# Optimization experiments

Measured on AMD Instinct MI355X. Metric: run time of the kernel, lower is better.

Reference implementation:

```python
import jax, jax.numpy as jnp
import numpy as np


def conv3d(x, w, b, stride=(1, 1, 1)):
    # x: (B,C,D,H,W), w: (O,I,3,3,3), padding 1 on all three dims (PyTorch Conv3d k=3,p=1)
    y = jax.lax.conv_general_dilated(
        x, w, stride, [(1, 1)] * 3,
        dimension_numbers=("NCDHW", "OIDHW", "NCDHW"))
    return y + b[None, :, None, None, None]


def deconv3d(x, w, b):
    # ConvTranspose3d with k=3, s=1, p=1 == conv with spatially flipped kernel
    return conv3d(x, jnp.flip(w, axis=(2, 3, 4)), b)


def upsample2x(x):
    # nn.Upsample(scale_factor=(1,2,2), mode='nearest')
    return jnp.repeat(jnp.repeat(x, 2, axis=3), 2, axis=4)


def fo_pool(z, f, reverse):
    # linear gated recurrence h_t = f_t*h_{t-1} + (1-f_t)*z_t along band axis (dim 2)
    zt = jnp.moveaxis(z, 2, 0)
    ft = jnp.moveaxis(f, 2, 0)
    if reverse:
        zt, ft = zt[::-1], ft[::-1]

    def step(h, zf):
        zi, fi = zf
        h = fi * h + (1.0 - fi) * zi
        return h, h

    _, hs = jax.lax.scan(step, jnp.zeros_like(zt[0]), (zt, ft))
    if reverse:
        hs = hs[::-1]
    return jnp.moveaxis(hs, 0, 2)


def qrnn(gates, reverse):
    z, f = jnp.split(gates, 2, axis=1)
    return fo_pool(jnp.tanh(z), jax.nn.sigmoid(f), reverse)


def biqrnn(gates):
    z, f1, f2 = jnp.split(gates, 3, axis=1)
    z = jnp.tanh(z)
    return (fo_pool(z, jax.nn.sigmoid(f1), False)
            + fo_pool(z, jax.nn.sigmoid(f2), True))


def _forward(x, fe_w, fe_b, e0_w, e0_b, e1_w, e1_b, e2_w, e2_b, e3_w, e3_b,
             e4_w, e4_b, d0_w, d0_b, d1_w, d1_b, d2_w, d2_b, d3_w, d3_b,
             d4_w, d4_b, rec_w, rec_b):
    # feature extractor: BiQRNNConv3D(1 -> 16), gates 48ch
    fe = biqrnn(conv3d(x, fe_w, fe_b))                        # (B,16,31,256,256)
    # encoder (alternating direction: F,T,F,T,F)
    e0 = qrnn(conv3d(fe, e0_w, e0_b), False)                  # 16ch @256
    e1 = qrnn(conv3d(e0, e1_w, e1_b, stride=(1, 2, 2)), True) # 32ch @128
    e2 = qrnn(conv3d(e1, e2_w, e2_b), False)                  # 32ch @128
    e3 = qrnn(conv3d(e2, e3_w, e3_b, stride=(1, 2, 2)), True) # 64ch @64
    e4 = qrnn(conv3d(e3, e4_w, e4_b), False)                  # 64ch @64
    # decoder (reverse starts at True after encoder toggles)
    d0 = qrnn(deconv3d(e4, d0_w, d0_b), True)                 # 64ch @64
    d1 = qrnn(conv3d(upsample2x(d0 + e3), d1_w, d1_b), False) # 32ch @128
    d2 = qrnn(deconv3d(d1 + e2, d2_w, d2_b), True)            # 32ch @128
    d3 = qrnn(conv3d(upsample2x(d2 + e1), d3_w, d3_b), False) # 16ch @256
    d4 = qrnn(deconv3d(d3 + e0, d4_w, d4_b), True)            # 16ch @256
    out = d4 + fe
    # reconstructor: BiQRNNDeConv3D(16 -> 1), act='tanh'
    out = biqrnn(deconv3d(out, rec_w, rec_b))                 # (B,1,31,256,256)
    return out + x


def setup_inputs() -> dict:
    key = jax.random.key(0)
    ks = jax.random.split(key, 26)

    def W(k, o, i):
        return jax.random.normal(k, (o, i, 3, 3, 3), jnp.float32) * 0.05

    def Bv(k, o):
        return jax.random.normal(k, (o,), jnp.float32) * 0.01

    x = jax.random.normal(ks[0], (1, 1, 31, 256, 256), jnp.float32)
    inp = {"x": x}
    shapes = {
        "fe": (48, 1), "e0": (32, 16), "e1": (64, 16), "e2": (64, 32),
        "e3": (128, 32), "e4": (128, 64), "d0": (128, 64), "d1": (64, 64),
        "d2": (64, 32), "d3": (32, 32), "d4": (32, 16), "rec": (3, 16),
    }
    for j, (name, (o, i)) in enumerate(shapes.items()):
        inp[name + "_w"] = W(ks[1 + 2 * j], o, i)
        inp[name + "_b"] = Bv(ks[2 + 2 * j], o)
    return inp


def reference(x, fe_w, fe_b, e0_w, e0_b, e1_w, e1_b, e2_w, e2_b, e3_w, e3_b,
              e4_w, e4_b, d0_w, d0_b, d1_w, d1_b, d2_w, d2_b, d3_w, d3_b,
              d4_w, d4_b, rec_w, rec_b):
    return _forward(x, fe_w, fe_b, e0_w, e0_b, e1_w, e1_b, e2_w, e2_b,
                    e3_w, e3_b, e4_w, e4_b, d0_w, d0_b, d1_w, d1_b,
                    d2_w, d2_b, d3_w, d3_b, d4_w, d4_b, rec_w, rec_b)
```

## Files before the change

### kernel.cpp

```cpp
#include <hip/hip_runtime.h>
#include <hip/hip_bf16.h>
#include <cstdint>
#include <cstddef>

using f16 = _Float16;
typedef _Float16 f16x2 __attribute__((ext_vector_type(2)));
typedef _Float16 f16x8 __attribute__((ext_vector_type(8)));
typedef float f32x4 __attribute__((ext_vector_type(4)));

static constexpr int DD = 31;
static constexpr long long U  = 31LL * 256 * 256;
static constexpr long long V2 = 31LL * 128 * 128;
static constexpr long long POOL_UNITS = 56;
static constexpr int CP_CHUNK = 16;

union U32H2 { unsigned u; f16x2 h; };

__device__ __forceinline__ float toF(float v) { return v; }
__device__ __forceinline__ float toF(f16 v) { return (float)v; }
__device__ __forceinline__ void stv(float* p, float v) { *p = v; }
__device__ __forceinline__ void stv(f16* p, float v) { *p = (f16)v; }
__device__ __forceinline__ float sigm(float x) { return 1.f / (1.f + __expf(-x)); }

__device__ __forceinline__ unsigned packh2(float a, float b)
{
    U32H2 r; r.h = f16x2{(f16)a, (f16)b}; return r.u;
}
__device__ __forceinline__ unsigned addh2(unsigned a, unsigned b)
{
    U32H2 x, y, r; x.u = a; y.u = b; r.h = x.h + y.h; return r.u;
}
__device__ __forceinline__ float dot2f(unsigned v, unsigned w, float c)
{
#if __has_builtin(__builtin_amdgcn_fdot2)
    U32H2 uv, uw; uv.u = v; uw.u = w;
    return __builtin_amdgcn_fdot2(uv.h, uw.h, c, false);
#else
    U32H2 uv, uw; uv.u = v; uw.u = w;
    c = fmaf((float)uv.h.x, (float)uw.h.x, c);
    return fmaf((float)uv.h.y, (float)uw.h.y, c);
#endif
}

__global__ __launch_bounds__(256)
void fill_k(f16* p, long long n)
{
    const long long stride = (long long)gridDim.x * 256;
    for (long long i = (long long)blockIdx.x * 256 + threadIdx.x; i < n; i += stride)
        p[i] = (f16)0.f;
}

__global__ __launch_bounds__(256)
void pack_w_k(const float* __restrict__ wt, f16* __restrict__ outp,
              int CIN, int nCo, int flip)
{
    const int e = blockIdx.x * 256 + threadIdx.x;
    const int nhg = (nCo + 7) >> 3;
    const int total = (CIN >> 3) * nhg * 9 * 64;
    if (e >= total) return;
    const int l = e & 63;
    const int r = e >> 6;
    const int r9 = r % 9;
    const int t2 = r / 9;
    const int hg = t2 % nhg;
    const int cc = t2 / nhg;
    const int kd = r9 / 3, Tg = r9 - kd * 3;
    const int n = hg * 8 + (l & 15);
    const int T = Tg * 4 + (l >> 4);
    f16x8 bv;
#pragma unroll
    for (int i = 0; i < 8; ++i) bv[i] = (f16)0.f;
    if (T <= 8 && n < nCo) {
        const int kh = T / 3, kw = T - (T / 3) * 3;
        const int st = flip ? ((2 - kd) * 9 + (2 - kh) * 3 + (2 - kw))
                            : (kd * 9 + kh * 3 + kw);
        const size_t wb8 = ((size_t)n * CIN + cc * 8) * 27 + st;
#pragma unroll
        for (int i = 0; i < 8; ++i)
            bv[i] = (f16)wt[wb8 + (size_t)i * 27];
    }
    *(f16x8*)(outp + (size_t)e * 8) = bv;
}

template<int STRIDE, bool FLIP, int CIN, int HOUT, int WOUT, int NT, bool PACKED,
         bool OUTIL>
__global__ __launch_bounds__(256)
void conv_mfma_k(const f16* __restrict__ in, const float* __restrict__ wt,
                 const f16x8* __restrict__ wb, const float* __restrict__ bias,
                 f16* __restrict__ out, int nCo, int cg0, int nhg)
{
    constexpr int CIC = CIN / 8;
    constexpr int HIN = HOUT * STRIDE, WIN = WOUT * STRIDE;
    constexpr int WT = (WOUT > 128) ? 128 : WOUT;
    constexpr int RR = 128 / WT;
    constexpr int COLS = WOUT / WT;
    constexpr int TPD = (HOUT / RR) * COLS;
    constexpr int AH = STRIDE * (RR - 1) + 3;
    constexpr int AW = STRIDE * (WT - 1) + 3;
    constexpr int APOS = 3 * AH * AW;
    constexpr int NBENT = NT * 576;

    extern __shared__ unsigned lds[];
    unsigned* Alds = lds;
    unsigned* Blds = lds + APOS * 4;

    const int tid = threadIdx.x;
    const int l = tid & 63;
    const int wid = tid >> 6;

    const int bx = blockIdx.x;
    const int d0 = bx / TPD;
    const int rem = bx - d0 * TPD;
    const int h0 = (rem / COLS) * RR;
    const int wb_ = (rem % COLS) * WT;

    const int co_base = blockIdx.y * (16 * NT);
    const int nRem = nCo - co_base;
    const int hgBase = cg0 + blockIdx.y * (2 * NT);

    const int base_h = STRIDE * h0 - 1;
    const int base_w = STRIDE * wb_ - 1;
    constexpr size_t HWin = (size_t)HIN * WIN;
    constexpr size_t DHW = (size_t)DD * HWin;
    const unsigned* inu = (const unsigned*)in;

    int hho[2], wlo[2];
#pragma unroll
    for (int mt = 0; mt < 2; ++mt) {
        const int p = wid * 32 + mt * 16 + (l & 15);
        hho[mt] = p / WT;
        wlo[mt] = p - hho[mt] * WT;
    }
    const int g = l >> 4;
    int khg[3], kwg[3];
#pragma unroll
    for (int Tg = 0; Tg < 3; ++Tg) {
        int T = Tg * 4 + g;
        if (T > 8) T = 8;
        khg[Tg] = T / 3;
        kwg[Tg] = T - (T / 3) * 3;
    }

    f32x4 acc[2][NT];
#pragma unroll
    for (int mt = 0; mt < 2; ++mt)
#pragma unroll
        for (int nt = 0; nt < NT; ++nt)
            acc[mt][nt] = (f32x4){0.f, 0.f, 0.f, 0.f};

    for (int cc = 0; cc < CIC; ++cc) {
        f16x8 bfr[NT][9];
        if (PACKED) {
#pragma unroll
            for (int nt = 0; nt < NT; ++nt)
#pragma unroll
                for (int r9 = 0; r9 < 9; ++r9)
                    bfr[nt][r9] = wb[((size_t)cc * nhg + hgBase + nt * 2) * 9 * 64
                                     + (size_t)r9 * 64 + l];
        }
        __syncthreads();
        for (int t = tid; t < APOS; t += 256) {
            const int ww = t % AW;
            const int t2 = t / AW;
            const int hh = t2 % AH;
            const int dd = t2 / AH;
            const int d = d0 - 1 + dd;
            const int h = base_h + hh;
            const int w = base_w + ww;
            uint4 val = make_uint4(0u, 0u, 0u, 0u);
            if ((unsigned)d < (unsigned)DD && (unsigned)h < (unsigned)HIN &&
                (unsigned)w < (unsigned)WIN) {
                const size_t gi = (size_t)(cc * 4) * DHW +
                                  (size_t)d * HWin + (size_t)h * WIN + w;
                val.x = inu[gi];
                val.y = inu[gi + DHW];
                val.z = inu[gi + 2 * DHW];
                val.w = inu[gi + 3 * DHW];
            }
            *(uint4*)(Alds + (size_t)t * 4) = val;
        }
        if (!PACKED) {
            for (int t = tid; t < NBENT; t += 256) {
                const int ll = t & 63;
                const int f = t >> 6;
                const int nt = f / 9;
                const int r9 = f - nt * 9;
                const int kd = r9 / 3;
                const int Tg = r9 - kd * 3;
                const int n = nt * 16 + (ll & 15);
                const int gg = ll >> 4;
                const int T = Tg * 4 + gg;
                f16x8 bv;
                if (T <= 8 && n < nRem) {
                    const int kh = T / 3, kw = T - (T / 3) * 3;
                    const int st = FLIP ? ((2 - kd) * 9 + (2 - kh) * 3 + (2 - kw))
                                        : (kd * 9 + kh * 3 + kw);
                    const size_t wb8 = ((size_t)(co_base + n) * CIN + cc * 8) * 27 + st;
#pragma unroll
                    for (int e = 0; e < 8; ++e)
                        bv[e] = (f16)wt[wb8 + (size_t)e * 27];
                } else {
#pragma unroll
                    for (int e = 0; e < 8; ++e) bv[e] = (f16)0.f;
                }
                *(f16x8*)(Blds + (size_t)t * 4) = bv;
            }
        }
        __syncthreads();
#pragma unroll
        for (int kd = 0; kd < 3; ++kd) {
#pragma unroll
            for (int Tg = 0; Tg < 3; ++Tg) {
                f16x8 bfrag[NT];
#pragma unroll
                for (int nt = 0; nt < NT; ++nt)
                    bfrag[nt] = PACKED ? bfr[nt][kd * 3 + Tg]
                                       : *(const f16x8*)
                        (Blds + (size_t)(((nt * 9) + kd * 3 + Tg) * 64 + l) * 4);
                const int kh = khg[Tg], kw = kwg[Tg];
#pragma unroll
                for (int mt = 0; mt < 2; ++mt) {
                    const int hh = STRIDE * hho[mt] + kh;
                    const int ww = STRIDE * wlo[mt] + kw;
                    const f16x8 afrag = *(const f16x8*)
                        (Alds + (size_t)((kd * AH + hh) * AW + ww) * 4);
#pragma unroll
                    for (int nt = 0; nt < NT; ++nt)
                        acc[mt][nt] = __builtin_amdgcn_mfma_f32_16x16x32_f16(
                            afrag, bfrag[nt], acc[mt][nt], 0, 0, 0);
                }
            }
        }
    }

    const int n = l & 15;
#pragma unroll
    for (int nt = 0; nt < NT; ++nt) {
        const int ng = nt * 16 + n;
        if (ng < nRem) {
            const int co = co_base + ng;
            const float bv = bias[co];
#pragma unroll
            for (int mt = 0; mt < 2; ++mt) {
#pragma unroll
                for (int r = 0; r < 4; ++r) {
                    const int p = wid * 32 + mt * 16 + (l >> 4) * 4 + r;
                    const int hh = p / WT;
                    const int wl = p - hh * WT;
                    const int h = h0 + hh, w = wb_ + wl;
                    const float val = acc[mt][nt][r] + bv;
                    if (OUTIL) {
                        const size_t coPlane =
                            (size_t)(co >> 1) * DD * HOUT * WOUT * 2 + (co & 1);
                        out[coPlane + ((size_t)d0 * HOUT + h) * WOUT * 2 +
                            (size_t)w * 2] = (f16)val;
                    } else {
                        out[((size_t)co * DD + d0) * HOUT * WOUT +
                            (size_t)h * WOUT + w] = (f16)val;
                    }
                }
            }
        }
    }
}

template<int CIN, int HLO, int WLO, int NT>
__global__ __launch_bounds__(256)
void conv_mfma_up_k(const f16* __restrict__ ia, const f16* __restrict__ ib,
                    const f16x8* __restrict__ wb, const float* __restrict__ bias,
                    f16* __restrict__ out, int nCo, int cg0, int nhg)
{
    constexpr int CIC = CIN / 8;
    constexpr int HOUT = 2 * HLO, WOUT = 2 * WLO;
    constexpr int WT = (WOUT > 128) ? 128 : WOUT;
    constexpr int COLS = WOUT / WT;
    constexpr int TPD = HOUT * COLS;
    constexpr int AWLO = WT / 2 + 2;
    constexpr int APOS = 3 * 2 * AWLO;

    extern __shared__ unsigned lds[];

    const int tid = threadIdx.x;
    const int l = tid & 63;
    const int wid = tid >> 6;

    const int bx = blockIdx.x;
    const int d0 = bx / TPD;
    const int rem = bx - d0 * TPD;
    const int h0 = rem / COLS;
    const int wb_ = (rem % COLS) * WT;

    const int co_base = blockIdx.y * (16 * NT);
    const int nRem = nCo - co_base;
    const int hgBase = cg0 + blockIdx.y * (2 * NT);

    const int rlo0 = (h0 - 1) >> 1;
    const int clo0 = (wb_ >> 1) - 1;

    constexpr size_t HWlo = (size_t)HLO * WLO;
    constexpr size_t DHW = (size_t)DD * HWlo;
    const unsigned* iau = (const unsigned*)ia;
    const unsigned* ibu = (const unsigned*)ib;

    int wpos[2];
#pragma unroll
    for (int mt = 0; mt < 2; ++mt)
        wpos[mt] = wid * 32 + mt * 16 + (l & 15);

    const int g = l >> 4;
    int khg[3], kwg[3];
#pragma unroll
    for (int Tg = 0; Tg < 3; ++Tg) {
        int T = Tg * 4 + g;
        if (T > 8) T = 8;
        khg[Tg] = T / 3;
        kwg[Tg] = T - (T / 3) * 3;
    }

    f32x4 acc[2][NT];
#pragma unroll
    for (int mt = 0; mt < 2; ++mt)
#pragma unroll
        for (int nt = 0; nt < NT; ++nt)
            acc[mt][nt] = (f32x4){0.f, 0.f, 0.f, 0.f};

    for (int cc = 0; cc < CIC; ++cc) {
        f16x8 bfr[NT][9];
#pragma unroll
        for (int nt = 0; nt < NT; ++nt)
#pragma unroll
            for (int r9 = 0; r9 < 9; ++r9)
                bfr[nt][r9] = wb[((size_t)cc * nhg + hgBase + nt * 2) * 9 * 64
                                 + (size_t)r9 * 64 + l];
        __syncthreads();
        for (int t = tid; t < APOS; t += 256) {
            const int ww = t % AWLO;
            const int t2 = t / AWLO;
            const int rr = t2 & 1;
            const int dd = t2 >> 1;
            const int d = d0 - 1 + dd;
            const int hlo = rlo0 + rr;
            const int wlo = clo0 + ww;
            uint4 val = make_uint4(0u, 0u, 0u, 0u);
            if ((unsigned)d < (unsigned)DD && (unsigned)hlo < (unsigned)HLO &&
                (unsigned)wlo < (unsigned)WLO) {
                const size_t gi = (size_t)(cc * 4) * DHW +
                                  (size_t)d * HWlo + (size_t)hlo * WLO + wlo;
                val.x = addh2(iau[gi], ibu[gi]);
                val.y = addh2(iau[gi + DHW], ibu[gi + DHW]);
                val.z = addh2(iau[gi + 2 * DHW], ibu[gi + 2 * DHW]);
                val.w = addh2(iau[gi + 3 * DHW], ibu[gi + 3 * DHW]);
            }
            *(uint4*)(lds + (size_t)t * 4) = val;
        }
        __syncthreads();
#pragma unroll
        for (int kd = 0; kd < 3; ++kd) {
#pragma unroll
            for (int Tg = 0; Tg < 3; ++Tg) {
                const int kh = khg[Tg], kw = kwg[Tg];
                const int rr = ((h0 + kh - 1) >> 1) - rlo0;
#pragma unroll
                for (int mt = 0; mt < 2; ++mt) {
                    const int iw = ((wpos[mt] + kw - 1) >> 1) + 1;
                    const f16x8 afrag = *(const f16x8*)
                        (lds + (size_t)((kd * 2 + rr) * AWLO + iw) * 4);
#pragma unroll
                    for (int nt = 0; nt < NT; ++nt)
                        acc[mt][nt] = __builtin_amdgcn_mfma_f32_16x16x32_f16(
                            afrag, bfr[nt][kd * 3 + Tg], acc[mt][nt], 0, 0, 0);
                }
            }
        }
    }

    const int n = l & 15;
#pragma unroll
    for (int nt = 0; nt < NT; ++nt) {
        const int ng = nt * 16 + n;
        if (ng < nRem) {
            const int co = co_base + ng;
            const float bv = bias[co];
            const size_t coPlane = (size_t)(co >> 1) * DD * HOUT * WOUT * 2 + (co & 1);
#pragma unroll
            for (int mt = 0; mt < 2; ++mt) {
#pragma unroll
                for (int r = 0; r < 4; ++r) {
                    const int p = wid * 32 + mt * 16 + (l >> 4) * 4 + r;
                    out[coPlane + ((size_t)d0 * HOUT + h0) * WOUT * 2 +
                        (size_t)(wb_ + p) * 2] = (f16)(acc[mt][nt][r] + bv);
                }
            }
        }
    }
}

template<int STRIDE, bool FLIP, int CO_BLK, bool OUT_IL>
__global__ __launch_bounds__(256, 2)
void conv3d_il_k(const f16* __restrict__ in, const float* __restrict__ wt,
                 const float* __restrict__ bias, f16* __restrict__ out,
                 int Cin, int Hin, int Win, int Hout, int Wout)
{
    extern __shared__ unsigned wl2[];
    const int co_base = blockIdx.y * CO_BLK;

    const int s8 = (blockIdx.x * 256 + threadIdx.x) * 8;
    const int w0 = s8 % Wout;
    const int sh = s8 / Wout;
    const int h0 = sh % Hout;
    const int d0 = sh / Hout;

    float acc[CO_BLK][8];
#pragma unroll
    for (int j = 0; j < CO_BLK; ++j) {
        const float bv = bias[co_base + j];
#pragma unroll
        for (int o = 0; o < 8; ++o) acc[j][o] = bv;
    }

    const size_t HWin = (size_t)Hin * Win;
    const int CP = Cin >> 1;

    for (int cp0 = 0; cp0 < CP; cp0 += CP_CHUNK) {
        const int cnp = (CP - cp0 < CP_CHUNK) ? (CP - cp0) : CP_CHUNK;
        __syncthreads();
        for (int t = threadIdx.x; t < cnp * 27 * CO_BLK; t += 256) {
            const int j = t % CO_BLK;
            const int k = (t / CO_BLK) % 27;
            const int cp = t / (CO_BLK * 27);
            int src;
            if (FLIP) {
                const int kd = k / 9, kh = (k / 3) % 3, kw = k % 3;
                src = (2 - kd) * 9 + (2 - kh) * 3 + (2 - kw);
            } else {
                src = k;
            }
            const int ci = (cp0 + cp) * 2;
            const size_t wb = (size_t)(co_base + j) * Cin;
            wl2[t] = packh2(wt[(wb + ci) * 27 + src], wt[(wb + ci + 1) * 27 + src]);
        }
        __syncthreads();

        for (int cp = 0; cp < cnp; ++cp) {
            const f16* cb = in + (size_t)(cp0 + cp) * DD * HWin * 2;
            const unsigned* wc = wl2 + cp * 27 * CO_BLK;
#pragma unroll
            for (int kd = 0; kd < 3; ++kd) {
                const int di = d0 + kd - 1;
                if (di < 0 || di >= DD) continue;
#pragma unroll
                for (int kh = 0; kh < 3; ++kh) {
                    const int hi = h0 * STRIDE + kh - 1;
                    if (hi < 0 || hi >= Hin) continue;
                    const unsigned* rowu = (const unsigned*)
                        (cb + ((size_t)di * HWin + (size_t)hi * Win) * 2);
                    if (STRIDE == 1) {
                        unsigned v2[10];
                        v2[0] = (w0 > 0) ? rowu[w0 - 1] : 0u;
                        const uint4 q1 = *(const uint4*)(rowu + w0);
                        const uint4 q2 = *(const uint4*)(rowu + w0 + 4);
                        v2[1] = q1.x; v2[2] = q1.y; v2[3] = q1.z; v2[4] = q1.w;
                        v2[5] = q2.x; v2[6] = q2.y; v2[7] = q2.z; v2[8] = q2.w;
                        v2[9] = (w0 + 8 < Win) ? rowu[w0 + 8] : 0u;
                        const unsigned* wk = wc + (kd * 9 + kh * 3) * CO_BLK;
#pragma unroll
                        for (int kw = 0; kw < 3; ++kw) {
#pragma unroll
                            for (int j = 0; j < CO_BLK; ++j) {
                                const unsigned wv = wk[kw * CO_BLK + j];
#pragma unroll
                                for (int o = 0; o < 8; ++o)
                                    acc[j][o] = dot2f(v2[o + kw], wv, acc[j][o]);
                            }
                        }
                    } else {
                        unsigned v2[17];
                        const int p0 = w0 * 2;
                        v2[0] = (w0 > 0) ? rowu[p0 - 1] : 0u;
#pragma unroll
                        for (int q = 0; q < 4; ++q) {
                            const uint4 qq = *(const uint4*)(rowu + p0 + 4 * q);
                            v2[1 + 4 * q] = qq.x; v2[2 + 4 * q] = qq.y;
                            v2[3 + 4 * q] = qq.z; v2[4 + 4 * q] = qq.w;
                        }
                        const unsigned* wk = wc + (kd * 9 + kh * 3) * CO_BLK;
#pragma unroll
                        for (int kw = 0; kw < 3; ++kw) {
#pragma unroll
                            for (int j = 0; j < CO_BLK; ++j) {
                                const unsigned wv = wk[kw * CO_BLK + j];
#pragma unroll
                                for (int o = 0; o < 8; ++o)
                                    acc[j][o] = dot2f(v2[2 * o + kw], wv, acc[j][o]);
                            }
                        }
                    }
                }
            }
        }
    }

    if (OUT_IL) {
#pragma unroll
        for (int pj = 0; pj < CO_BLK / 2; ++pj) {
            f16* op = out + ((((size_t)((co_base >> 1) + pj) * DD + d0) * Hout + h0)
                             * Wout + w0) * 2;
            unsigned dw[8];
#pragma unroll
            for (int o = 0; o < 8; ++o)
                dw[o] = packh2(acc[2 * pj][o], acc[2 * pj + 1][o]);
            *(uint4*)op = make_uint4(dw[0], dw[1], dw[2], dw[3]);
            *(uint4*)(op + 8) = make_uint4(dw[4], dw[5], dw[6], dw[7]);
        }
    } else {
#pragma unroll
        for (int j = 0; j < CO_BLK; ++j) {
            f16* op = out + (((size_t)(co_base + j) * DD + d0) * Hout + h0) * Wout + w0;
            unsigned dw[4];
#pragma unroll
            for (int o = 0; o < 4; ++o)
                dw[o] = packh2(acc[j][2 * o], acc[j][2 * o + 1]);
            *(uint4*)op = make_uint4(dw[0], dw[1], dw[2], dw[3]);
        }
    }
}

template<int CO_BLK>
__global__ __launch_bounds__(256, 2)
void conv3d_up_il_k(const f16* __restrict__ ia, const f16* __restrict__ ib,
                    const float* __restrict__ wt, const float* __restrict__ bias,
                    f16* __restrict__ out, int Cin, int Hlo, int Wlo)
{
    extern __shared__ unsigned wl2[];
    const int co_base = blockIdx.y * CO_BLK;

    const int Hout = 2 * Hlo, Wout = 2 * Wlo;
    const int s8 = (blockIdx.x * 256 + threadIdx.x) * 8;
    const int w0 = s8 % Wout;
    const int sh = s8 / Wout;
    const int h0 = sh % Hout;
    const int d0 = sh / Hout;
    const int lw = w0 >> 1;

    float acc[CO_BLK][8];
#pragma unroll
    for (int j = 0; j < CO_BLK; ++j) {
        const float bv = bias[co_base + j];
#pragma unroll
        for (int o = 0; o < 8; ++o) acc[j][o] = bv;
    }
    const size_t HWlo = (size_t)Hlo * Wlo;
    const int CP = Cin >> 1;

    for (int cp0 = 0; cp0 < CP; cp0 += CP_CHUNK) {
        const int cnp = (CP - cp0 < CP_CHUNK) ? (CP - cp0) : CP_CHUNK;
        __syncthreads();
        for (int t = threadIdx.x; t < cnp * 27 * CO_BLK; t += 256) {
            const int j = t % CO_BLK;
            const int k = (t / CO_BLK) % 27;
            const int cp = t / (CO_BLK * 27);
            const int ci = (cp0 + cp) * 2;
            const size_t wb = (size_t)(co_base + j) * Cin;
            wl2[t] = packh2(wt[(wb + ci) * 27 + k], wt[(wb + ci + 1) * 27 + k]);
        }
        __syncthreads();

        for (int cp = 0; cp < cnp; ++cp) {
            const f16* cba = ia + (size_t)(cp0 + cp) * DD * HWlo * 2;
            const f16* cbb = ib + (size_t)(cp0 + cp) * DD * HWlo * 2;
            const unsigned* wc = wl2 + cp * 27 * CO_BLK;
#pragma unroll
            for (int kd = 0; kd < 3; ++kd) {
                const int di = d0 + kd - 1;
                if (di < 0 || di >= DD) continue;
#pragma unroll
                for (int kh = 0; kh < 3; ++kh) {
                    const int hi = h0 + kh - 1;
                    if (hi < 0 || hi >= Hout) continue;
                    const int hlo = hi >> 1;
                    const unsigned* rua = (const unsigned*)
                        (cba + ((size_t)di * HWlo + (size_t)hlo * Wlo) * 2);
                    const unsigned* rub = (const unsigned*)
                        (cbb + ((size_t)di * HWlo + (size_t)hlo * Wlo) * 2);
                    unsigned u[6];
                    u[0] = (lw > 0) ? addh2(rua[lw - 1], rub[lw - 1]) : 0u;
                    const uint4 qa = *(const uint4*)(rua + lw);
                    const uint4 qb = *(const uint4*)(rub + lw);
                    u[1] = addh2(qa.x, qb.x); u[2] = addh2(qa.y, qb.y);
                    u[3] = addh2(qa.z, qb.z); u[4] = addh2(qa.w, qb.w);
                    u[5] = (lw + 4 < Wlo) ? addh2(rua[lw + 4], rub[lw + 4]) : 0u;
                    const unsigned v2[10] = { u[0], u[1], u[1], u[2], u[2],
                                              u[3], u[3], u[4], u[4], u[5] };
                    const unsigned* wk = wc + (kd * 9 + kh * 3) * CO_BLK;
#pragma unroll
                    for (int kw = 0; kw < 3; ++kw) {
#pragma unroll
                        for (int j = 0; j < CO_BLK; ++j) {
                            const unsigned wv = wk[kw * CO_BLK + j];
#pragma unroll
                            for (int o = 0; o < 8; ++o)
                                acc[j][o] = dot2f(v2[o + kw], wv, acc[j][o]);
                        }
                    }
                }
            }
        }
    }
#pragma unroll
    for (int pj = 0; pj < CO_BLK / 2; ++pj) {
        f16* op = out + ((((size_t)((co_base >> 1) + pj) * DD + d0) * Hout + h0)
                         * Wout + w0) * 2;
        unsigned dw[8];
#pragma unroll
        for (int o = 0; o < 8; ++o)
            dw[o] = packh2(acc[2 * pj][o], acc[2 * pj + 1][o]);
        *(uint4*)op = make_uint4(dw[0], dw[1], dw[2], dw[3]);
        *(uint4*)(op + 8) = make_uint4(dw[4], dw[5], dw[6], dw[7]);
    }
}

__global__ __launch_bounds__(256, 2)
void conv_fe_k(const float* __restrict__ in, const float* __restrict__ wt,
               const float* __restrict__ bias, f16* __restrict__ out)
{
    __shared__ float wl[27 * 4];
    for (int t = threadIdx.x; t < 27 * 4; t += 256) {
        const int j = t % 4;
        const int k = t / 4;
        wl[t] = wt[(size_t)j * 27 + k];
    }
    __syncthreads();

    const int W = 256, H = 256;
    const int s8 = (blockIdx.x * 256 + threadIdx.x) * 8;
    const int w0 = s8 % W;
    const int sh = s8 / W;
    const int h0 = sh % H;
    const int d0 = sh / H;

    float acc[4][8];
#pragma unroll
    for (int j = 0; j < 4; ++j) {
        const float bv = bias[j];
#pragma unroll
        for (int o = 0; o < 8; ++o) acc[j][o] = bv;
    }
    const size_t HW = 65536;

#pragma unroll
    for (int kd = 0; kd < 3; ++kd) {
        const int di = d0 + kd - 1;
        if (di < 0 || di >= DD) continue;
#pragma unroll
        for (int kh = 0; kh < 3; ++kh) {
            const int hi = h0 + kh - 1;
            if (hi < 0 || hi >= H) continue;
            const float* row = in + (size_t)di * HW + (size_t)hi * W + w0;
            float v[10];
            v[0] = (w0 > 0) ? row[-1] : 0.f;
            const float4 q1 = *(const float4*)row;
            const float4 q2 = *(const float4*)(row + 4);
            v[1] = q1.x; v[2] = q1.y; v[3] = q1.z; v[4] = q1.w;
            v[5] = q2.x; v[6] = q2.y; v[7] = q2.z; v[8] = q2.w;
            v[9] = (w0 + 8 < W) ? row[8] : 0.f;
            const float* wk = wl + (kd * 9 + kh * 3) * 4;
#pragma unroll
            for (int kw = 0; kw < 3; ++kw) {
#pragma unroll
                for (int j = 0; j < 4; ++j) {
                    const float wv = wk[kw * 4 + j];
#pragma unroll
                    for (int o = 0; o < 8; ++o)
                        acc[j][o] = fmaf(v[o + kw], wv, acc[j][o]);
                }
            }
        }
    }
#pragma unroll
    for (int pj = 0; pj < 2; ++pj) {
        f16* op = out + (((size_t)pj * DD + d0) * H + h0) * (size_t)W * 2 + (size_t)w0 * 2;
        unsigned dw[8];
#pragma unroll
        for (int o = 0; o < 8; ++o)
            dw[o] = packh2(acc[2 * pj][o], acc[2 * pj + 1][o]);
        *(uint4*)op = make_uint4(dw[0], dw[1], dw[2], dw[3]);
        *(uint4*)(op + 8) = make_uint4(dw[4], dw[5], dw[6], dw[7]);
    }
}

template<bool IL, typename TA1, typename TA2, typename TO>
__global__ __launch_bounds__(256)
void fo_pool_k(const f16* __restrict__ z, const f16* __restrict__ f,
               TO* __restrict__ out, const TA1* __restrict__ a1,
               const TA2* __restrict__ a2, int C, int HW, int reverse)
{
    const long long idx = (long long)blockIdx.x * 256 + threadIdx.x;
    if (idx >= (long long)C * HW) return;
    size_t base; size_t step;
    if (IL) {
        const long long pairIdx = idx / (2LL * HW);
        const int rem = (int)(idx - pairIdx * 2LL * HW);
        const int p = rem >> 1;
        const int par = rem & 1;
        base = ((size_t)pairIdx * DD * HW + p) * 2 + par;
        step = (size_t)HW * 2;
    } else {
        const int c = (int)(idx / HW);
        const int p = (int)(idx - (long long)c * HW);
        base = (size_t)c * DD * HW + p;
        step = (size_t)HW;
    }
    float h = 0.f;
    if (!reverse) {
        for (int d = 0; d < DD; ++d) {
            const size_t off = base + (size_t)d * step;
            const float zz = tanhf(toF(z[off]));
            const float ff = sigm(toF(f[off]));
            h = ff * h + (1.f - ff) * zz;
            float v = h;
            if (a1) v += toF(a1[off]);
            if (a2) v += toF(a2[off]);
            stv(out + off, v);
        }
    } else {
        for (int d = DD - 1; d >= 0; --d) {
            const size_t off = base + (size_t)d * step;
            const float zz = tanhf(toF(z[off]));
            const float ff = sigm(toF(f[off]));
            h = ff * h + (1.f - ff) * zz;
            float v = h;
            if (a1) v += toF(a1[off]);
            if (a2) v += toF(a2[off]);
            stv(out + off, v);
        }
    }
}

__global__ __launch_bounds__(256)
void diag_k(float* out, float v, int n)
{
    const int i = blockIdx.x * 256 + threadIdx.x;
    if (i < n) out[i] = v;
}


template<int STRIDE, bool FLIP, int CIN, int HOUT, int WOUT, int NT, bool PACKED,
         bool OUTIL>
static inline void mfma_launch(const f16* in, const float* w, const f16x8* wb,
                               const float* b, f16* out, int co0, int nCo,
                               int nhg, hipStream_t s)
{
    constexpr int WT = WOUT > 128 ? 128 : WOUT;
    constexpr int RR = 128 / WT;
    constexpr int AH = STRIDE * (RR - 1) + 3;
    constexpr int AW = STRIDE * (WT - 1) + 3;
    constexpr size_t lds = (size_t)(3 * AH * AW) * 16 +
                           (PACKED ? 0 : (size_t)NT * 9216);
    dim3 grid((unsigned)(DD * (HOUT / RR) * (WOUT / WT)),
              (unsigned)((nCo + 16 * NT - 1) / (16 * NT)));
    conv_mfma_k<STRIDE, FLIP, CIN, HOUT, WOUT, NT, PACKED, OUTIL>
        <<<grid, 256, lds, s>>>(
        in, w + (size_t)co0 * CIN * 27, wb, b + co0, out, nCo, co0 / 8, nhg);
}

template<int CIN, int HLO, int WLO, int NT>
static inline void mfma_up_launch(const f16* ia, const f16* ib, const f16x8* wb,
                                  const float* b, f16* out, int co0, int nCo,
                                  int nhg, hipStream_t s)
{
    constexpr int WOUT = 2 * WLO;
    constexpr int WT = WOUT > 128 ? 128 : WOUT;
    constexpr int AWLO = WT / 2 + 2;
    constexpr size_t lds = (size_t)(3 * 2 * AWLO) * 16;
    dim3 grid((unsigned)(DD * (2 * HLO) * (WOUT / WT)),
              (unsigned)((nCo + 16 * NT - 1) / (16 * NT)));
    conv_mfma_up_k<CIN, HLO, WLO, NT><<<grid, 256, lds, s>>>(
        ia, ib, wb, b + co0, out, nCo, co0 / 8, nhg);
}

static inline void conv_launch(const f16* in, const float* w, const float* b,
                               f16* out, int Cin, int co0, int nCo,
                               int Hin, int Win, int Hout, int Wout,
                               int stride, bool flip, hipStream_t s)
{
    const unsigned gx = (unsigned)((DD * (long long)Hout * Wout) / 2048);
    const float* wp = w + (size_t)co0 * Cin * 27;
    const float* bp = b + co0;
    const int cpc = (Cin / 2 < CP_CHUNK) ? Cin / 2 : CP_CHUNK;
    if (flip) {
        if (nCo % 4 == 0) {
            dim3 grid(gx, nCo / 4);
            conv3d_il_k<1, true, 4, true><<<grid, 256, (size_t)cpc * 27 * 4 * 4, s>>>(
                in, wp, bp, out, Cin, Hin, Win, Hout, Wout);
        } else {
            dim3 grid(gx, 1);
            conv3d_il_k<1, true, 3, false><<<grid, 256, (size_t)cpc * 27 * 3 * 4, s>>>(
                in, wp, bp, out, Cin, Hin, Win, Hout, Wout);
        }
    } else {
        dim3 grid(gx, nCo / 8);
        conv3d_il_k<1, false, 8, true><<<grid, 256, (size_t)cpc * 27 * 8 * 4, s>>>(
            in, wp, bp, out, Cin, Hin, Win, Hout, Wout);
    }
}

static inline void conv_up_launch(const f16* ia, const f16* ib, const float* w,
                                  const float* b, f16* out, int Cin, int co0,
                                  int nCo, int Hlo, int Wlo, hipStream_t s)
{
    const unsigned gx = (unsigned)((DD * 4LL * Hlo * Wlo) / 2048);
    const int cpc = (Cin / 2 < CP_CHUNK) ? Cin / 2 : CP_CHUNK;
    if (nCo % 8 == 0) {
        dim3 grid(gx, nCo / 8);
        conv3d_up_il_k<8><<<grid, 256, (size_t)cpc * 27 * 8 * 4, s>>>(
            ia, ib, w + (size_t)co0 * Cin * 27, b + co0, out, Cin, Hlo, Wlo);
    } else {
        dim3 grid(gx, nCo / 4);
        conv3d_up_il_k<4><<<grid, 256, (size_t)cpc * 27 * 4 * 4, s>>>(
            ia, ib, w + (size_t)co0 * Cin * 27, b + co0, out, Cin, Hlo, Wlo);
    }
}

template<bool IL, typename TA1, typename TA2, typename TO>
static inline void pool_launch(const f16* z, const f16* f, TO* o, const TA1* a1,
                               const TA2* a2, int C, int HW, int rev,
                               hipStream_t s)
{
    const long long tot = (long long)C * HW;
    fo_pool_k<IL, TA1, TA2, TO><<<(unsigned)((tot + 255) / 256), 256, 0, s>>>(
        z, f, o, a1, a2, C, HW, rev);
}

static inline void pack_launch(const float* w, f16* outp, int CIN, int nCo,
                               int flip, hipStream_t s)
{
    const int total = (CIN / 8) * ((nCo + 7) / 8) * 9 * 64;
    pack_w_k<<<(total + 255) / 256, 256, 0, s>>>(w, outp, CIN, nCo, flip);
}

static constexpr size_t pk_sz(int CIN, int nCo)
{ return (size_t)(CIN / 8) * ((nCo + 7) / 8) * 9 * 64 * 8; }

static void run_net(const float* x, const float* const* W, const float* const* B,
                    float* out, f16* P, bool packed, hipStream_t s)
{
    const f16* np = nullptr;
    const float* npf = nullptr;

    f16* WP = P + 56 * U;
    f16* PK_e0 = WP;
    f16* PK_e1 = PK_e0 + pk_sz(16, 32);
    f16* PK_e2 = PK_e1 + pk_sz(16, 64);
    f16* PK_e3 = PK_e2 + pk_sz(32, 64);
    f16* PK_e4 = PK_e3 + pk_sz(32, 128);
    f16* PK_d0 = PK_e4 + pk_sz(64, 128);
    f16* PK_d2 = PK_d0 + pk_sz(64, 128);
    f16* PK_d1 = PK_d0;
    f16* PK_d3 = PK_d1 + pk_sz(64, 64);
    f16* PK_d4 = PK_d3 + pk_sz(32, 32);
    f16* PK_rec = PK_d4 + pk_sz(16, 32);
    if (packed) {
        pack_launch(W[1], PK_e0, 16, 32, 0, s);
        pack_launch(W[2], PK_e1, 16, 64, 0, s);
        pack_launch(W[3], PK_e2, 32, 64, 0, s);
        pack_launch(W[4], PK_e3, 32, 128, 0, s);
        pack_launch(W[5], PK_e4, 64, 128, 0, s);
        pack_launch(W[6], PK_d0, 64, 128, 1, s);
        pack_launch(W[8], PK_d2, 32, 64, 1, s);
    }

#define MFMA_CALL(S, F, CI, H, Wd, NTv, in_, wt_, wb_, bi_, out_, co0_, nco_, nhg_) \
    do { if (packed) mfma_launch<S, F, CI, H, Wd, NTv, true, true>(in_, wt_, (const f16x8*)(wb_), bi_, out_, co0_, nco_, nhg_, s); \
         else        mfma_launch<S, F, CI, H, Wd, NTv, false, true>(in_, wt_, nullptr, bi_, out_, co0_, nco_, nhg_, s); } while (0)

    fill_k<<<2048, 256, 0, s>>>(P, POOL_UNITS * U);

    f16* FE = P + 32 * U;
    for (int a = 0; a < 16; a += 4) {
        conv_fe_k<<<992, 256, 0, s>>>(x, W[0] + (size_t)a * 27,        B[0] + a,      P);
        conv_fe_k<<<992, 256, 0, s>>>(x, W[0] + (size_t)(16 + a) * 27, B[0] + 16 + a, P + 4 * U);
        conv_fe_k<<<992, 256, 0, s>>>(x, W[0] + (size_t)(32 + a) * 27, B[0] + 32 + a, P + 8 * U);
        pool_launch<true, f16, float, f16>(P, P + 4 * U, P + 12 * U, np, npf, 4, 65536, 0, s);
        pool_launch<true, f16, float, f16>(P, P + 8 * U, FE + (size_t)a * U, P + 12 * U, npf, 4, 65536, 1, s);
    }

    f16* E0 = P + 16 * U;
    MFMA_CALL(1, false, 16, 256, 256, 1, FE, W[1], PK_e0, B[1], P, 0, 16, 4);
    for (int a = 0; a < 16; a += 8) {
        f16* G = P + 48 * U;
        MFMA_CALL(1, false, 16, 256, 256, 1, FE, W[1], PK_e0, B[1], G, 16 + a, 8, 4);
        pool_launch<true, f16, float, f16>(P + (size_t)a * U, G, E0 + (size_t)a * U,
                                           np, npf, 8, 65536, 0, s);
    }

    f16* E1 = P;
    {
        f16* G = P + 32 * U;
        MFMA_CALL(2, false, 16, 128, 128, 2, E0, W[2], PK_e1, B[2], G, 0, 64, 8);
        pool_launch<true, f16, float, f16>(G, G + 8 * U, E1, np, npf, 32, 16384, 1, s);
    }

    f16* E2 = P + 8 * U;
    {
        f16* G = P + 32 * U;
        MFMA_CALL(1, false, 32, 128, 128, 2, E1, W[3], PK_e2, B[3], G, 0, 64, 8);
        pool_launch<true, f16, float, f16>(G, G + 8 * U, E2, np, npf, 32, 16384, 0, s);
    }

    f16* E3 = P + 32 * U;
    {
        f16* G = P + 48 * U;
        MFMA_CALL(2, false, 32, 64, 64, 2, E2, W[4], PK_e3, B[4], G, 0, 128, 16);
        pool_launch<true, f16, float, f16>(G, G + 4 * U, E3, np, npf, 64, 4096, 1, s);
    }

    f16* E4 = P + 40 * U;
    {
        f16* G = P + 48 * U;
        MFMA_CALL(1, false, 64, 64, 64, 2, E3, W[5], PK_e4, B[5], G, 0, 128, 16);
        pool_launch<true, f16, float, f16>(G, G + 4 * U, E4, np, npf, 64, 4096, 0, s);
    }

    f16* D0 = P + 44 * U;
    {
        f16* G = P + 48 * U;
        MFMA_CALL(1, true, 64, 64, 64, 2, E4, W[6], PK_d0, B[6], G, 0, 128, 16);
        pool_launch<true, f16, float, f16>(G, G + 4 * U, D0, np, npf, 64, 4096, 1, s);
    }
    if (packed) {
        pack_launch(W[7],  PK_d1, 64, 64, 0, s);
        pack_launch(W[9],  PK_d3, 32, 32, 0, s);
        pack_launch(W[10], PK_d4, 16, 32, 1, s);
        pack_launch(W[11], PK_rec, 16, 3, 1, s);
    }

    f16* D1 = P + 36 * U;
    for (int a = 0; a < 32; a += 16) {
        f16* G = P + 48 * U;
        if (packed) {
            mfma_up_launch<64, 64, 64, 1>(D0, E3, (const f16x8*)PK_d1, B[7], G,
                                          a, 16, 8, s);
            mfma_up_launch<64, 64, 64, 1>(D0, E3, (const f16x8*)PK_d1, B[7], G + 4 * U,
                                          32 + a, 16, 8, s);
        } else {
            conv_up_launch(D0, E3, W[7], B[7], G,         64, a,      16, 64, 64, s);
            conv_up_launch(D0, E3, W[7], B[7], G + 4 * U, 64, 32 + a, 16, 64, 64, s);
        }
        pool_launch<true, f16, float, f16>(G, G + 4 * U, D1 + (size_t)a * V2,
                                           E2 + (size_t)a * V2, npf, 16, 16384, 0, s);
    }

    f16* D2 = P + 8 * U;
    for (int a = 0; a < 32; a += 16) {
        f16* G = P + 48 * U;
        MFMA_CALL(1, true, 32, 128, 128, 1, D1, W[8], PK_d2, B[8], G,         a,      16, 8);
        MFMA_CALL(1, true, 32, 128, 128, 1, D1, W[8], PK_d2, B[8], G + 4 * U, 32 + a, 16, 8);
        pool_launch<true, f16, float, f16>(G, G + 4 * U, D2 + (size_t)a * V2, np, npf, 16, 16384, 1, s);
    }

    f16* D3 = P + 32 * U;
    if (packed) {
        f16* G = P + 48 * U;
        mfma_up_launch<32, 128, 128, 1>(D2, E1, (const f16x8*)PK_d3, B[9], D3,
                                        0, 16, 4, s);
        for (int a = 0; a < 16; a += 8) {
            mfma_up_launch<32, 128, 128, 1>(D2, E1, (const f16x8*)PK_d3, B[9], G,
                                            16 + a, 8, 4, s);
            pool_launch<true, f16, float, f16>(D3 + (size_t)a * U, G,
                                               D3 + (size_t)a * U,
                                               E0 + (size_t)a * U, npf, 8, 65536, 0, s);
        }
    } else {
        for (int a = 0; a < 16; a += 4) {
            f16* G = P + 48 * U;
            conv_up_launch(D2, E1, W[9], B[9], G,         32, a,      4, 128, 128, s);
            conv_up_launch(D2, E1, W[9], B[9], G + 4 * U, 32, 16 + a, 4, 128, 128, s);
            pool_launch<true, f16, float, f16>(G, G + 4 * U, D3 + (size_t)a * U,
                                               E0 + (size_t)a * U, npf, 4, 65536, 0, s);
        }
    }

    f16* FE2 = P;
    for (int a = 0; a < 16; a += 4) {
        f16* G = P + 16 * U;
        conv_fe_k<<<992, 256, 0, s>>>(x, W[0] + (size_t)a * 27,        B[0] + a,      G);
        conv_fe_k<<<992, 256, 0, s>>>(x, W[0] + (size_t)(16 + a) * 27, B[0] + 16 + a, G + 4 * U);
        conv_fe_k<<<992, 256, 0, s>>>(x, W[0] + (size_t)(32 + a) * 27, B[0] + 32 + a, G + 8 * U);
        pool_launch<true, f16, float, f16>(G, G + 4 * U, G + 12 * U, np, npf, 4, 65536, 0, s);
        pool_launch<true, f16, float, f16>(G, G + 8 * U, FE2 + (size_t)a * U, G + 12 * U, npf, 4, 65536, 1, s);
    }

    f16* D4 = P + 16 * U;
    if (packed) {
        f16* G = P + 48 * U;
        mfma_launch<1, true, 16, 256, 256, 1, true, true>(
            D3, W[10], (const f16x8*)PK_d4, B[10], D4, 0, 16, 4, s);
        for (int a = 0; a < 16; a += 8) {
            mfma_launch<1, true, 16, 256, 256, 1, true, true>(
                D3, W[10], (const f16x8*)PK_d4, B[10], G, 16 + a, 8, 4, s);
            pool_launch<true, f16, float, f16>(D4 + (size_t)a * U, G,
                                               D4 + (size_t)a * U,
                                               FE2 + (size_t)a * U, npf, 8, 65536, 1, s);
        }
    } else {
        for (int a = 0; a < 16; a += 4) {
            f16* G = P + 48 * U;
            conv_launch(D3, W[10], B[10], G,         16, a,      4, 256, 256, 256, 256, 1, true, s);
            conv_launch(D3, W[10], B[10], G + 4 * U, 16, 16 + a, 4, 256, 256, 256, 256, 1, true, s);
            pool_launch<true, f16, float, f16>(G, G + 4 * U, D4 + (size_t)a * U,
                                               FE2 + (size_t)a * U, npf, 4, 65536, 1, s);
        }
    }

    {
        f16* G = P + 32 * U;
        f16* TMP = P + 35 * U;
        if (packed) {
            mfma_launch<1, true, 16, 256, 256, 1, true, false>(
                D4, W[11], (const f16x8*)PK_rec, B[11], G, 0, 3, 1, s);
        } else {
            conv_launch(D4, W[11], B[11], G, 16, 0, 3, 256, 256, 256, 256, 1, true, s);
        }
        pool_launch<false, f16, float, f16>(G, G + 1 * U, TMP, np, npf, 1, 65536, 0, s);
        pool_launch<false, f16, float, float>(G, G + 2 * U, out, TMP, x, 1, 65536, 1, s);
    }
#undef MFMA_CALL
}

extern "C" void kernel_launch(void* const* d_in, const int* in_sizes, int n_in,
                              void* d_out, int out_size, void* d_ws, size_t ws_size,
                              hipStream_t stream)
{
    const float* x = (const float*)d_in[0];
    const float* W[12];
    const float* B[12];
    for (int i = 0; i < 12; ++i) {
        W[i] = (const float*)d_in[1 + 2 * i];
        B[i] = (const float*)d_in[2 + 2 * i];
    }

    const size_t need_base = (size_t)(POOL_UNITS * U) * sizeof(f16);
    const size_t need_pack = (size_t)(57 * U) * sizeof(f16);
    if (ws_size >= need_pack) {
        run_net(x, W, B, (float*)d_out, (f16*)d_ws, true, stream);
    } else if (ws_size >= need_base) {
        run_net(x, W, B, (float*)d_out, (f16*)d_ws, false, stream);
    } else {
        const float ws_mb = (float)((double)ws_size / 1048576.0);
        diag_k<<<(out_size + 255) / 256, 256, 0, stream>>>(
            (float*)d_out, ws_mb, out_size);
    }
}
```

Before: 4.531 ms.

## Merge conv launches with split-output NT=2 and pre-add skip connections

The 256x256 e0/d4 convs and the d3 upsample conv now compute 24 output channels in one NT=2 launch, routing channels past a split index to a separate gate buffer. This replaces three launches per layer with two and reuses each input tile across more channels. The skip-connection sum is moved out of the upsample conv's tile load into a separate vectorised add kernel that runs once before the conv, so repeated conv launches no longer re-read both inputs. The upsample LDS row stride is padded by one entry to reduce bank conflicts. The trade-offs are an extra full-tensor add pass, higher register pressure from NT=2, and the add now overwrites D0 and D2 in place.

```diff
diff --git a/kernel.cpp b/kernel.cpp
--- a/kernel.cpp
+++ b/kernel.cpp
@@ -13,6 +13,7 @@
 static constexpr long long V2 = 31LL * 128 * 128;
 static constexpr long long POOL_UNITS = 56;
 static constexpr int CP_CHUNK = 16;
+static constexpr int COSPLIT_NONE = 1 << 30;
 
 union U32H2 { unsigned u; f16x2 h; };
 
@@ -48,6 +49,18 @@
     const long long stride = (long long)gridDim.x * 256;
     for (long long i = (long long)blockIdx.x * 256 + threadIdx.x; i < n; i += stride)
         p[i] = (f16)0.f;
+}
+
+__global__ __launch_bounds__(256)
+void add_k(f16* __restrict__ a, const f16* __restrict__ b, long long n8)
+{
+    const long long i = (long long)blockIdx.x * 256 + threadIdx.x;
+    if (i >= n8) return;
+    uint4 va = ((const uint4*)a)[i];
+    const uint4 vb = ((const uint4*)b)[i];
+    va.x = addh2(va.x, vb.x); va.y = addh2(va.y, vb.y);
+    va.z = addh2(va.z, vb.z); va.w = addh2(va.w, vb.w);
+    ((uint4*)a)[i] = va;
 }
 
 __global__ __launch_bounds__(256)
@@ -87,7 +100,8 @@
 __global__ __launch_bounds__(256)
 void conv_mfma_k(const f16* __restrict__ in, const float* __restrict__ wt,
                  const f16x8* __restrict__ wb, const float* __restrict__ bias,
-                 f16* __restrict__ out, int nCo, int cg0, int nhg)
+                 f16* __restrict__ out, f16* __restrict__ outF, int coSplit,
+                 int nCo, int cg0, int nhg)
 {
     constexpr int CIC = CIN / 8;
     constexpr int HIN = HOUT * STRIDE, WIN = WOUT * STRIDE;
@@ -240,6 +254,9 @@
         if (ng < nRem) {
             const int co = co_base + ng;
             const float bv = bias[co];
+            f16* dst = out;
+            int cs = co;
+            if (OUTIL && co >= coSplit) { dst = outF; cs = co - coSplit; }
 #pragma unroll
             for (int mt = 0; mt < 2; ++mt) {
 #pragma unroll
@@ -251,8 +268,8 @@
                     const float val = acc[mt][nt][r] + bv;
                     if (OUTIL) {
                         const size_t coPlane =
-                            (size_t)(co >> 1) * DD * HOUT * WOUT * 2 + (co & 1);
-                        out[coPlane + ((size_t)d0 * HOUT + h) * WOUT * 2 +
+                            (size_t)(cs >> 1) * DD * HOUT * WOUT * 2 + (cs & 1);
+                        dst[coPlane + ((size_t)d0 * HOUT + h) * WOUT * 2 +
                             (size_t)w * 2] = (f16)val;
                     } else {
                         out[((size_t)co * DD + d0) * HOUT * WOUT +
@@ -266,9 +283,10 @@
 
 template<int CIN, int HLO, int WLO, int NT>
 __global__ __launch_bounds__(256)
-void conv_mfma_up_k(const f16* __restrict__ ia, const f16* __restrict__ ib,
-                    const f16x8* __restrict__ wb, const float* __restrict__ bias,
-                    f16* __restrict__ out, int nCo, int cg0, int nhg)
+void conv_mfma_up_k(const f16* __restrict__ in, const f16x8* __restrict__ wb,
+                    const float* __restrict__ bias, f16* __restrict__ out,
+                    f16* __restrict__ outF, int coSplit,
+                    int nCo, int cg0, int nhg)
 {
     constexpr int CIC = CIN / 8;
     constexpr int HOUT = 2 * HLO, WOUT = 2 * WLO;
@@ -276,6 +294,7 @@
     constexpr int COLS = WOUT / WT;
     constexpr int TPD = HOUT * COLS;
     constexpr int AWLO = WT / 2 + 2;
+    constexpr int AWLOP = AWLO + 1;
     constexpr int APOS = 3 * 2 * AWLO;
 
     extern __shared__ unsigned lds[];
@@ -299,8 +318,7 @@
 
     constexpr size_t HWlo = (size_t)HLO * WLO;
     constexpr size_t DHW = (size_t)DD * HWlo;
-    const unsigned* iau = (const unsigned*)ia;
-    const unsigned* ibu = (const unsigned*)ib;
+    const unsigned* inu = (const unsigned*)in;
 
     int wpos[2];
 #pragma unroll
@@ -346,12 +364,12 @@
                 (unsigned)wlo < (unsigned)WLO) {
                 const size_t gi = (size_t)(cc * 4) * DHW +
                                   (size_t)d * HWlo + (size_t)hlo * WLO + wlo;
-                val.x = addh2(iau[gi], ibu[gi]);
-                val.y = addh2(iau[gi + DHW], ibu[gi + DHW]);
-                val.z = addh2(iau[gi + 2 * DHW], ibu[gi + 2 * DHW]);
-                val.w = addh2(iau[gi + 3 * DHW], ibu[gi + 3 * DHW]);
+                val.x = inu[gi];
+                val.y = inu[gi + DHW];
+                val.z = inu[gi + 2 * DHW];
+                val.w = inu[gi + 3 * DHW];
             }
-            *(uint4*)(lds + (size_t)t * 4) = val;
+            *(uint4*)(lds + (size_t)((dd * 2 + rr) * AWLOP + ww) * 4) = val;
         }
         __syncthreads();
 #pragma unroll
@@ -364,7 +382,7 @@
                 for (int mt = 0; mt < 2; ++mt) {
                     const int iw = ((wpos[mt] + kw - 1) >> 1) + 1;
                     const f16x8 afrag = *(const f16x8*)
-                        (lds + (size_t)((kd * 2 + rr) * AWLO + iw) * 4);
+                        (lds + (size_t)((kd * 2 + rr) * AWLOP + iw) * 4);
 #pragma unroll
                     for (int nt = 0; nt < NT; ++nt)
                         acc[mt][nt] = __builtin_amdgcn_mfma_f32_16x16x32_f16(
@@ -381,13 +399,16 @@
         if (ng < nRem) {
             const int co = co_base + ng;
             const float bv = bias[co];
-            const size_t coPlane = (size_t)(co >> 1) * DD * HOUT * WOUT * 2 + (co & 1);
+            f16* dst = out;
+            int cs = co;
+            if (co >= coSplit) { dst = outF; cs = co - coSplit; }
+            const size_t coPlane = (size_t)(cs >> 1) * DD * HOUT * WOUT * 2 + (cs & 1);
 #pragma unroll
             for (int mt = 0; mt < 2; ++mt) {
 #pragma unroll
                 for (int r = 0; r < 4; ++r) {
                     const int p = wid * 32 + mt * 16 + (l >> 4) * 4 + r;
-                    out[coPlane + ((size_t)d0 * HOUT + h0) * WOUT * 2 +
+                    dst[coPlane + ((size_t)d0 * HOUT + h0) * WOUT * 2 +
                         (size_t)(wb_ + p) * 2] = (f16)(acc[mt][nt][r] + bv);
                 }
             }
@@ -747,8 +768,8 @@
 template<int STRIDE, bool FLIP, int CIN, int HOUT, int WOUT, int NT, bool PACKED,
          bool OUTIL>
 static inline void mfma_launch(const f16* in, const float* w, const f16x8* wb,
-                               const float* b, f16* out, int co0, int nCo,
-                               int nhg, hipStream_t s)
+                               const float* b, f16* out, f16* outF, int coSplit,
+                               int co0, int nCo, int nhg, hipStream_t s)
 {
     constexpr int WT = WOUT > 128 ? 128 : WOUT;
     constexpr int RR = 128 / WT;
@@ -760,22 +781,24 @@
               (unsigned)((nCo + 16 * NT - 1) / (16 * NT)));
     conv_mfma_k<STRIDE, FLIP, CIN, HOUT, WOUT, NT, PACKED, OUTIL>
         <<<grid, 256, lds, s>>>(
-        in, w + (size_t)co0 * CIN * 27, wb, b + co0, out, nCo, co0 / 8, nhg);
+        in, w + (size_t)co0 * CIN * 27, wb, b + co0, out, outF, coSplit,
+        nCo, co0 / 8, nhg);
 }
 
 template<int CIN, int HLO, int WLO, int NT>
-static inline void mfma_up_launch(const f16* ia, const f16* ib, const f16x8* wb,
-                                  const float* b, f16* out, int co0, int nCo,
+static inline void mfma_up_launch(const f16* in, const f16x8* wb,
+                                  const float* b, f16* out, f16* outF,
+                                  int coSplit, int co0, int nCo,
                                   int nhg, hipStream_t s)
 {
     constexpr int WOUT = 2 * WLO;
     constexpr int WT = WOUT > 128 ? 128 : WOUT;
-    constexpr int AWLO = WT / 2 + 2;
-    constexpr size_t lds = (size_t)(3 * 2 * AWLO) * 16;
+    constexpr int AWLOP = WT / 2 + 3;
+    constexpr size_t lds = (size_t)(3 * 2 * AWLOP) * 16;
     dim3 grid((unsigned)(DD * (2 * HLO) * (WOUT / WT)),
               (unsigned)((nCo + 16 * NT - 1) / (16 * NT)));
     conv_mfma_up_k<CIN, HLO, WLO, NT><<<grid, 256, lds, s>>>(
-        ia, ib, wb, b + co0, out, nCo, co0 / 8, nhg);
+        in, wb, b + co0, out, outF, coSplit, nCo, co0 / 8, nhg);
 }
 
 static inline void conv_launch(const f16* in, const float* w, const float* b,
@@ -836,6 +859,12 @@
 {
     const int total = (CIN / 8) * ((nCo + 7) / 8) * 9 * 64;
     pack_w_k<<<(total + 255) / 256, 256, 0, s>>>(w, outp, CIN, nCo, flip);
+}
+
+static inline void add_launch(f16* a, const f16* b, long long n, hipStream_t s)
+{
+    const long long n8 = n / 8;
+    add_k<<<(unsigned)((n8 + 255) / 256), 256, 0, s>>>(a, b, n8);
 }
 
 static constexpr size_t pk_sz(int CIN, int nCo)
@@ -870,8 +899,8 @@
     }
 
 #define MFMA_CALL(S, F, CI, H, Wd, NTv, in_, wt_, wb_, bi_, out_, co0_, nco_, nhg_) \
-    do { if (packed) mfma_launch<S, F, CI, H, Wd, NTv, true, true>(in_, wt_, (const f16x8*)(wb_), bi_, out_, co0_, nco_, nhg_, s); \
-         else        mfma_launch<S, F, CI, H, Wd, NTv, false, true>(in_, wt_, nullptr, bi_, out_, co0_, nco_, nhg_, s); } while (0)
+    do { if (packed) mfma_launch<S, F, CI, H, Wd, NTv, true, true>(in_, wt_, (const f16x8*)(wb_), bi_, out_, nullptr, COSPLIT_NONE, co0_, nco_, nhg_, s); \
+         else        mfma_launch<S, F, CI, H, Wd, NTv, false, true>(in_, wt_, nullptr, bi_, out_, nullptr, COSPLIT_NONE, co0_, nco_, nhg_, s); } while (0)
 
     fill_k<<<2048, 256, 0, s>>>(P, POOL_UNITS * U);
 
@@ -885,12 +914,23 @@
     }
 
     f16* E0 = P + 16 * U;
-    MFMA_CALL(1, false, 16, 256, 256, 1, FE, W[1], PK_e0, B[1], P, 0, 16, 4);
-    for (int a = 0; a < 16; a += 8) {
+    if (packed) {
         f16* G = P + 48 * U;
-        MFMA_CALL(1, false, 16, 256, 256, 1, FE, W[1], PK_e0, B[1], G, 16 + a, 8, 4);
-        pool_launch<true, f16, float, f16>(P + (size_t)a * U, G, E0 + (size_t)a * U,
-                                           np, npf, 8, 65536, 0, s);
+        mfma_launch<1, false, 16, 256, 256, 2, true, true>(
+            FE, W[1], (const f16x8*)PK_e0, B[1], P, G, 16, 0, 24, 4, s);
+        pool_launch<true, f16, float, f16>(P, G, E0, np, npf, 8, 65536, 0, s);
+        mfma_launch<1, false, 16, 256, 256, 1, true, true>(
+            FE, W[1], (const f16x8*)PK_e0, B[1], G, nullptr, COSPLIT_NONE,
+            24, 8, 4, s);
+        pool_launch<true, f16, float, f16>(P + 8 * U, G, E0 + 8 * U, np, npf, 8, 65536, 0, s);
+    } else {
+        MFMA_CALL(1, false, 16, 256, 256, 1, FE, W[1], PK_e0, B[1], P, 0, 16, 4);
+        for (int a = 0; a < 16; a += 8) {
+            f16* G = P + 48 * U;
+            MFMA_CALL(1, false, 16, 256, 256, 1, FE, W[1], PK_e0, B[1], G, 16 + a, 8, 4);
+            pool_launch<true, f16, float, f16>(P + (size_t)a * U, G, E0 + (size_t)a * U,
+                                               np, npf, 8, 65536, 0, s);
+        }
     }
 
     f16* E1 = P;
@@ -935,13 +975,15 @@
     }
 
     f16* D1 = P + 36 * U;
+    if (packed)
+        add_launch(D0, E3, 4 * U, s);
     for (int a = 0; a < 32; a += 16) {
         f16* G = P + 48 * U;
         if (packed) {
-            mfma_up_launch<64, 64, 64, 1>(D0, E3, (const f16x8*)PK_d1, B[7], G,
-                                          a, 16, 8, s);
-            mfma_up_launch<64, 64, 64, 1>(D0, E3, (const f16x8*)PK_d1, B[7], G + 4 * U,
-                                          32 + a, 16, 8, s);
+            mfma_up_launch<64, 64, 64, 1>(D0, (const f16x8*)PK_d1, B[7], G,
+                                          nullptr, COSPLIT_NONE, a, 16, 8, s);
+            mfma_up_launch<64, 64, 64, 1>(D0, (const f16x8*)PK_d1, B[7], G + 4 * U,
+                                          nullptr, COSPLIT_NONE, 32 + a, 16, 8, s);
         } else {
             conv_up_launch(D0, E3, W[7], B[7], G,         64, a,      16, 64, 64, s);
             conv_up_launch(D0, E3, W[7], B[7], G + 4 * U, 64, 32 + a, 16, 64, 64, s);
@@ -961,15 +1003,14 @@
     f16* D3 = P + 32 * U;
     if (packed) {
         f16* G = P + 48 * U;
-        mfma_up_launch<32, 128, 128, 1>(D2, E1, (const f16x8*)PK_d3, B[9], D3,
-                                        0, 16, 4, s);
-        for (int a = 0; a < 16; a += 8) {
-            mfma_up_launch<32, 128, 128, 1>(D2, E1, (const f16x8*)PK_d3, B[9], G,
-                                            16 + a, 8, 4, s);
-            pool_launch<true, f16, float, f16>(D3 + (size_t)a * U, G,
-                                               D3 + (size_t)a * U,
-                                               E0 + (size_t)a * U, npf, 8, 65536, 0, s);
-        }
+        add_launch(D2, E1, 8 * U, s);
+        mfma_up_launch<32, 128, 128, 2>(D2, (const f16x8*)PK_d3, B[9], D3,
+                                        G, 16, 0, 24, 4, s);
+        pool_launch<true, f16, float, f16>(D3, G, D3, E0, npf, 8, 65536, 0, s);
+        mfma_up_launch<32, 128, 128, 1>(D2, (const f16x8*)PK_d3, B[9], G,
+                                        nullptr, COSPLIT_NONE, 24, 8, 4, s);
+        pool_launch<true, f16, float, f16>(D3 + 8 * U, G, D3 + 8 * U,
+                                           E0 + 8 * U, npf, 8, 65536, 0, s);
     } else {
         for (int a = 0; a < 16; a += 4) {
             f16* G = P + 48 * U;
@@ -993,15 +1034,14 @@
     f16* D4 = P + 16 * U;
     if (packed) {
         f16* G = P + 48 * U;
+        mfma_launch<1, true, 16, 256, 256, 2, true, true>(
+            D3, W[10], (const f16x8*)PK_d4, B[10], D4, G, 16, 0, 24, 4, s);
+        pool_launch<true, f16, float, f16>(D4, G, D4, FE2, npf, 8, 65536, 1, s);
         mfma_launch<1, true, 16, 256, 256, 1, true, true>(
-            D3, W[10], (const f16x8*)PK_d4, B[10], D4, 0, 16, 4, s);
-        for (int a = 0; a < 16; a += 8) {
-            mfma_launch<1, true, 16, 256, 256, 1, true, true>(
-                D3, W[10], (const f16x8*)PK_d4, B[10], G, 16 + a, 8, 4, s);
-            pool_launch<true, f16, float, f16>(D4 + (size_t)a * U, G,
-                                               D4 + (size_t)a * U,
-                                               FE2 + (size_t)a * U, npf, 8, 65536, 1, s);
-        }
+            D3, W[10], (const f16x8*)PK_d4, B[10], G, nullptr, COSPLIT_NONE,
+            24, 8, 4, s);
+        pool_launch<true, f16, float, f16>(D4 + 8 * U, G, D4 + 8 * U,
+                                           FE2 + 8 * U, npf, 8, 65536, 1, s);
     } else {
         for (int a = 0; a < 16; a += 4) {
             f16* G = P + 48 * U;
@@ -1017,7 +1057,8 @@
         f16* TMP = P + 35 * U;
         if (packed) {
             mfma_launch<1, true, 16, 256, 256, 1, true, false>(
-                D4, W[11], (const f16x8*)PK_rec, B[11], G, 0, 3, 1, s);
+                D4, W[11], (const f16x8*)PK_rec, B[11], G, nullptr, COSPLIT_NONE,
+                0, 3, 1, s);
         } else {
             conv_launch(D4, W[11], B[11], G, 16, 0, 3, 256, 256, 256, 256, 1, true, s);
         }
```

After: 4.282 ms. 1.06x faster.
